# Performance work log

Hardware: AMD Instinct MI355X
Metric: run time of the kernel (lower is better)

## Reference

```python
import jax, jax.numpy as jnp
import numpy as np

B, F, V, D, K = 16384, 39, 30000, 16, 20
EPS = 1e-5


def bn_eval(x, g, b):
    # inference-mode BatchNorm1d with running_mean=0, running_var=1
    return g * x / jnp.sqrt(1.0 + EPS) + b


def setup_inputs() -> dict:
    key = jax.random.key(0)
    ks = jax.random.split(key, 12)
    x = jax.random.randint(ks[0], (B, F), 0, V)
    emb_table = jax.random.normal(ks[1], (F * V, D), dtype=jnp.float32) * 0.05
    w_c = jax.random.normal(ks[2], (F, F * D), dtype=jnp.float32) * 0.05
    w0 = jax.random.normal(ks[3], (1024, F * D), dtype=jnp.float32) * 0.04
    w1 = jax.random.normal(ks[4], (512, 1024), dtype=jnp.float32) * 0.03
    w_out = jax.random.normal(ks[5], (1, 512), dtype=jnp.float32) * 0.04
    return {
        'x': x, 'emb_table': emb_table,
        'w_c': w_c, 'b_c': jnp.zeros((F,)), 'g_c': jnp.ones((F,)), 'be_c': jnp.zeros((F,)),
        'w0': w0, 'b0': jnp.zeros((1024,)), 'g0': jnp.ones((1024,)), 'be0': jnp.zeros((1024,)),
        'w1': w1, 'b1': jnp.zeros((512,)), 'g1': jnp.ones((512,)), 'be1': jnp.zeros((512,)),
        'w_out': w_out, 'b_out': jnp.zeros((1,)),
    }


def reference(x, emb_table, w_c, b_c, g_c, be_c, w0, b0, g0, be0,
              w1, b1, g1, be1, w_out, b_out):
    offsets = jnp.arange(F, dtype=x.dtype) * V          # per-field offsets
    idx = x + offsets[None, :]                          # [B, F]
    emb = emb_table[idx]                                # [B, F, D] gather

    # controller_mlp: flatten (batch, D, F) layout like torch transpose(1,2)
    flat = jnp.transpose(emb, (0, 2, 1)).reshape(B, F * D)
    h = jax.nn.relu(bn_eval(flat @ w_c.T + b_c, g_c, be_c))
    scores = jax.nn.softmax(h, axis=1)                  # [B, F]

    # kmax_pooling: top-k field indices, sorted ascending, gather weights
    _, kidx = jax.lax.top_k(scores, K)
    kidx = jnp.sort(kidx, axis=1)                       # [B, K]
    w = jnp.take_along_axis(scores, kidx, axis=1)       # [B, K]

    # forward_select: gather selected field embeddings, weight them
    sel = jnp.take_along_axis(emb, kidx[:, :, None], axis=1)  # [B, K, D]
    weighted = sel * w[:, :, None]

    # scatter back into full field slots (unselected fields are zero)
    full = jnp.zeros((B, F, D), weighted.dtype)
    bidx = jnp.arange(B)[:, None]
    full = full.at[bidx, kidx].set(weighted)            # [B, F, D]

    z = jnp.transpose(full, (0, 2, 1)).reshape(B, F * D)
    z = jax.nn.relu(bn_eval(z @ w0.T + b0, g0, be0))
    z = jax.nn.relu(bn_eval(z @ w1.T + b1, g1, be1))
    out = jax.nn.sigmoid(z @ w_out.T + b_out)           # [B, 1]
    return out.squeeze(-1)
```

## Files before the change

kernel.cpp:

```cpp
#include <hip/hip_runtime.h>
#include <math.h>

#define B_SZ 16384
#define F_N 39
#define V_N 30000
#define D_N 16
#define K_SEL 20
#define FD 624
#define KP0 640
#define NCP 48
#define N0 1024
#define N1 512
#define CBR 16
#define ALD 648

typedef unsigned short u16;
typedef __attribute__((ext_vector_type(8))) short bf16x8;
typedef __attribute__((ext_vector_type(8))) unsigned short u16x8;
typedef __attribute__((ext_vector_type(4))) float f32x4;
typedef __attribute__((ext_vector_type(4))) unsigned short u16x4;

__device__ __forceinline__ u16 f2bf(float v) {
    union { float f; unsigned u; } x; x.f = v;
    unsigned r = x.u + 0x7fff + ((x.u >> 16) & 1);
    return (u16)(r >> 16);
}
__device__ __forceinline__ float bf2f(u16 v) {
    union { unsigned u; float f; } x; x.u = ((unsigned)v) << 16;
    return x.f;
}
__device__ __forceinline__ unsigned cvtpk2(float a, float b) {
    unsigned d;
    asm("v_cvt_pk_bf16_f32 %0, %1, %2" : "=v"(d) : "v"(a), "v"(b));
    return d;
}

#define GLD16(gp, lp) __builtin_amdgcn_global_load_lds( \
    (const __attribute__((address_space(1))) unsigned int*)(gp), \
    (__attribute__((address_space(3))) unsigned int*)(lp), 16, 0, 0)

#define PREP_W0 (N0 * KP0)
#define PREP_W1 (N1 * N0)
#define PREP_WC (NCP * KP0)
#define PREP_TOT (PREP_W0 + PREP_W1 + PREP_WC + 3 * NCP + B_SZ)

__global__ __launch_bounds__(256) void prep_all_kernel(
    const float* __restrict__ w0, const float* __restrict__ w1,
    const float* __restrict__ w_c, const float* __restrict__ b_c,
    const float* __restrict__ g_c, const float* __restrict__ be_c,
    u16* __restrict__ w0b, u16* __restrict__ w1b, u16* __restrict__ wcb,
    float* __restrict__ bcp, float* __restrict__ gcp, float* __restrict__ becp,
    float* __restrict__ outp)
{
    int i = blockIdx.x * blockDim.x + threadIdx.x;
    if (i < PREP_W0) {
        int n = i / KP0, kk = i - n * KP0;
        float v = 0.f;
        if (kk < FD) v = w0[n * FD + (kk & 15) * F_N + (kk >> 4)];
        w0b[i] = f2bf(v);
        return;
    }
    i -= PREP_W0;
    if (i < PREP_W1) { w1b[i] = f2bf(w1[i]); return; }
    i -= PREP_W1;
    if (i < PREP_WC) {
        int n = i / KP0, kk = i - n * KP0;
        float v = 0.f;
        if (n < F_N && kk < FD) v = w_c[n * FD + (kk & 15) * F_N + (kk >> 4)];
        wcb[i] = f2bf(v);
        return;
    }
    i -= PREP_WC;
    if (i < 3 * NCP) {
        int which = i / NCP, n = i - which * NCP;
        float v = 0.f;
        if (n < F_N) v = (which == 0) ? b_c[n] : (which == 1) ? g_c[n] : be_c[n];
        ((which == 0) ? bcp : (which == 1) ? gcp : becp)[n] = v;
        return;
    }
    i -= 3 * NCP;
    if (i < B_SZ) outp[i] = 0.f;
}

__global__ __launch_bounds__(256) void fused_controller_kernel(
    const int* __restrict__ x, const float* __restrict__ emb_table,
    const u16* __restrict__ wcb, const float* __restrict__ bcp,
    const float* __restrict__ gcp, const float* __restrict__ becp,
    u16* __restrict__ zb)
{
    __shared__ __align__(16) u16 Al[CBR * ALD];
    __shared__ float vv[CBR][49];
    __shared__ f32x4 part[4][64][3];
    __shared__ float selw[CBR][F_N];

    const int t    = threadIdx.x;
    const int wave = t >> 6;
    const int lane = t & 63;
    const int b0   = blockIdx.x * CBR;

    {
        const int p0 = t, p1 = t + 256, p2 = t + 512;
        const int xi0 = x[b0 * F_N + p0];
        const int xi1 = x[b0 * F_N + p1];
        const int xi2 = (p2 < CBR * F_N) ? x[b0 * F_N + p2] : 0;
        const int pp[3] = { p0, p1, p2 };
        const int xx[3] = { xi0, xi1, xi2 };
        #pragma unroll
        for (int s = 0; s < 3; ++s) {
            const int p = pp[s];
            if (p < CBR * F_N) {
                const int row = p / F_N;
                const int f   = p - row * F_N;
                const float4* src =
                    (const float4*)(emb_table + (size_t)(xx[s] + f * V_N) * D_N);
                float4 v0 = src[0], v1 = src[1], v2 = src[2], v3 = src[3];
                uint4 o0 = { cvtpk2(v0.x, v0.y), cvtpk2(v0.z, v0.w),
                             cvtpk2(v1.x, v1.y), cvtpk2(v1.z, v1.w) };
                uint4 o1 = { cvtpk2(v2.x, v2.y), cvtpk2(v2.z, v2.w),
                             cvtpk2(v3.x, v3.y), cvtpk2(v3.z, v3.w) };
                *(uint4*)&Al[row * ALD + f * D_N]     = o0;
                *(uint4*)&Al[row * ALD + f * D_N + 8] = o1;
            }
        }
    }
    __syncthreads();

    const int m = lane & 15;
    const int q = lane >> 4;
    f32x4 acc0 = {}, acc1 = {}, acc2 = {};
    {
        const u16* ap  = &Al[m * ALD + wave * 160 + q * 8];
        const u16* bp0 = wcb + (size_t)(0  + m) * KP0 + wave * 160 + q * 8;
        const u16* bp1 = wcb + (size_t)(16 + m) * KP0 + wave * 160 + q * 8;
        const u16* bp2 = wcb + (size_t)(32 + m) * KP0 + wave * 160 + q * 8;
        #pragma unroll
        for (int k = 0; k < 5; ++k) {
            bf16x8 af = *(const bf16x8*)ap;
            bf16x8 b0 = *(const bf16x8*)bp0;
            bf16x8 b1 = *(const bf16x8*)bp1;
            bf16x8 b2 = *(const bf16x8*)bp2;
            acc0 = __builtin_amdgcn_mfma_f32_16x16x32_bf16(af, b0, acc0, 0, 0, 0);
            acc1 = __builtin_amdgcn_mfma_f32_16x16x32_bf16(af, b1, acc1, 0, 0, 0);
            acc2 = __builtin_amdgcn_mfma_f32_16x16x32_bf16(af, b2, acc2, 0, 0, 0);
            ap += 32; bp0 += 32; bp1 += 32; bp2 += 32;
        }
    }
    part[wave][lane][0] = acc0;
    part[wave][lane][1] = acc1;
    part[wave][lane][2] = acc2;
    __syncthreads();

    {
        f32x4 r0 = part[0][lane][0] + part[1][lane][0] + part[2][lane][0] + part[3][lane][0];
        f32x4 r1 = part[0][lane][1] + part[1][lane][1] + part[2][lane][1] + part[3][lane][1];
        f32x4 r2 = part[0][lane][2] + part[1][lane][2] + part[2][lane][2] + part[3][lane][2];

        const float rs = rsqrtf(1.0f + 1e-5f);
        if (q == wave) {
            #pragma unroll
            for (int j = 0; j < 3; ++j) {
                const f32x4 a = (j == 0) ? r0 : (j == 1) ? r1 : r2;
                const int n = j * 16 + m;
                const float gn = gcp[n] * rs;
                const float bn = becp[n];
                const float bi = bcp[n];
                #pragma unroll
                for (int r = 0; r < 4; ++r)
                    vv[wave * 4 + r][n] = fmaxf(fmaf(gn, a[r] + bi, bn), 0.f);
            }
        }
    }
    __syncthreads();

    {
        const int row = wave * 4 + (lane >> 4);
        const int fl  = lane & 15;
        float e[3] = {0.f, 0.f, 0.f};
        float mloc = -1e30f;
        #pragma unroll
        for (int it = 0; it < 3; ++it) {
            const int f = fl + 16 * it;
            if (f < F_N) { e[it] = vv[row][f]; mloc = fmaxf(mloc, e[it]); }
        }
        mloc = fmaxf(mloc, __shfl_xor(mloc, 1, 64));
        mloc = fmaxf(mloc, __shfl_xor(mloc, 2, 64));
        mloc = fmaxf(mloc, __shfl_xor(mloc, 4, 64));
        mloc = fmaxf(mloc, __shfl_xor(mloc, 8, 64));
        float sloc = 0.f;
        #pragma unroll
        for (int it = 0; it < 3; ++it) {
            const int f = fl + 16 * it;
            if (f < F_N) { e[it] = expf(e[it] - mloc); sloc += e[it]; }
        }
        sloc += __shfl_xor(sloc, 1, 64);
        sloc += __shfl_xor(sloc, 2, 64);
        sloc += __shfl_xor(sloc, 4, 64);
        sloc += __shfl_xor(sloc, 8, 64);
        const float inv = 1.f / sloc;
        #pragma unroll
        for (int it = 0; it < 3; ++it) {
            const int f = fl + 16 * it;
            if (f < F_N) vv[row][f] = e[it];
        }

        int rank[3] = {};
        for (int gg = 0; gg < F_N; ++gg) {
            const float o = vv[row][gg];
            #pragma unroll
            for (int it = 0; it < 3; ++it) {
                const int f = fl + 16 * it;
                if (f < F_N)
                    rank[it] += (o > e[it] || (o == e[it] && gg < f)) ? 1 : 0;
            }
        }
        #pragma unroll
        for (int it = 0; it < 3; ++it) {
            const int f = fl + 16 * it;
            if (f < F_N)
                selw[row][f] = (rank[it] < K_SEL) ? e[it] * inv : 0.f;
        }
    }
    __syncthreads();

    for (int gp = t; gp < CBR * 40; gp += 256) {
        const int row  = gp / 40;
        const int slot = gp - row * 40;
        u16* dst = zb + (size_t)(b0 + row) * KP0 + slot * D_N;
        uint4 o0 = {0u,0u,0u,0u}, o1 = {0u,0u,0u,0u};
        if (slot < F_N) {
            const float w = selw[row][slot];
            u16x8 a0 = *(u16x8*)&Al[row * ALD + slot * D_N];
            u16x8 a1 = *(u16x8*)&Al[row * ALD + slot * D_N + 8];
            o0 = (uint4){ cvtpk2(bf2f(a0[0]) * w, bf2f(a0[1]) * w),
                          cvtpk2(bf2f(a0[2]) * w, bf2f(a0[3]) * w),
                          cvtpk2(bf2f(a0[4]) * w, bf2f(a0[5]) * w),
                          cvtpk2(bf2f(a0[6]) * w, bf2f(a0[7]) * w) };
            o1 = (uint4){ cvtpk2(bf2f(a1[0]) * w, bf2f(a1[1]) * w),
                          cvtpk2(bf2f(a1[2]) * w, bf2f(a1[3]) * w),
                          cvtpk2(bf2f(a1[4]) * w, bf2f(a1[5]) * w),
                          cvtpk2(bf2f(a1[6]) * w, bf2f(a1[7]) * w) };
        }
        *(uint4*)dst       = o0;
        *(uint4*)(dst + 8) = o1;
    }
}

template<int MODE>
__global__ __launch_bounds__(512) void gemm_mfma_bn_relu(
    const u16* __restrict__ A, const u16* __restrict__ W,
    const float* __restrict__ bias, const float* __restrict__ g,
    const float* __restrict__ be, u16* __restrict__ Cout,
    int M, int N, int Kp,
    const float* __restrict__ w_out, float* __restrict__ outp)
{
    __shared__ __align__(16) u16 SM[3 * 12288];

    const int t    = threadIdx.x;
    const int wave = t >> 6;
    const int lane = t & 63;
    const int wm   = wave >> 1, wn = wave & 1;
    const int m0   = blockIdx.x * 256;
    const int n0   = blockIdx.y * 128;

    const int rA0 = t >> 2;
    const int cA0 = (t & 3) ^ ((rA0 >> 1) & 3);
    const int rA1 = 128 + rA0;
    const int cA1 = (t & 3) ^ ((rA1 >> 1) & 3);
    const u16* gA0 = A + (size_t)(m0 + rA0) * Kp + cA0 * 8;
    const u16* gA1 = A + (size_t)(m0 + rA1) * Kp + cA1 * 8;
    const u16* gB  = W + (size_t)(n0 + rA0) * Kp + cA0 * 8;
    const int dA0 = t * 8, dA1 = 4096 + t * 8, dB = 8192 + t * 8;

    const int q    = lane >> 4;
    const int lr16 = lane & 15;

    int aoff[4], boff[4];
    #pragma unroll
    for (int i = 0; i < 4; ++i) {
        int ra = wm * 64 + i * 16 + lr16;
        aoff[i] = ra * 32 + ((q ^ ((ra >> 1) & 3)) * 8);
        int rb = wn * 64 + i * 16 + lr16;
        boff[i] = rb * 32 + ((q ^ ((rb >> 1) & 3)) * 8);
    }

    const int NIT = Kp >> 5;

    GLD16(gA0, SM + dA0);
    GLD16(gA1, SM + dA1);
    GLD16(gB,  SM + dB);
    gA0 += 32; gA1 += 32; gB += 32;
    GLD16(gA0, SM + 12288 + dA0);
    GLD16(gA1, SM + 12288 + dA1);
    GLD16(gB,  SM + 12288 + dB);
    gA0 += 32; gA1 += 32; gB += 32;

    f32x4 acc[4][4] = {};
    int cur = 0, stg = 2;

    for (int it = 0; it < NIT - 1; ++it) {
        asm volatile("s_waitcnt vmcnt(3)" ::: "memory");
        __builtin_amdgcn_s_barrier();
        __builtin_amdgcn_sched_barrier(0);

        if (it + 2 < NIT) {
            u16* s = SM + stg * 12288;
            GLD16(gA0, s + dA0);
            GLD16(gA1, s + dA1);
            GLD16(gB,  s + dB);
            gA0 += 32; gA1 += 32; gB += 32;
        }

        const u16* ac = SM + cur * 12288;
        const u16* bc = ac + 8192;
        bf16x8 af[4], bfr[4];
        #pragma unroll
        for (int i = 0; i < 4; ++i) af[i]  = *(const bf16x8*)(ac + aoff[i]);
        #pragma unroll
        for (int j = 0; j < 4; ++j) bfr[j] = *(const bf16x8*)(bc + boff[j]);

        __builtin_amdgcn_s_setprio(1);
        #pragma unroll
        for (int i = 0; i < 4; ++i)
            #pragma unroll
            for (int j = 0; j < 4; ++j)
                acc[i][j] = __builtin_amdgcn_mfma_f32_16x16x32_bf16(
                    af[i], bfr[j], acc[i][j], 0, 0, 0);
        __builtin_amdgcn_s_setprio(0);

        cur = (cur == 2) ? 0 : cur + 1;
        stg = (stg == 2) ? 0 : stg + 1;
    }

    asm volatile("s_waitcnt vmcnt(0)" ::: "memory");
    __builtin_amdgcn_s_barrier();
    __builtin_amdgcn_sched_barrier(0);
    {
        const u16* ac = SM + cur * 12288;
        const u16* bc = ac + 8192;
        bf16x8 af[4], bfr[4];
        #pragma unroll
        for (int i = 0; i < 4; ++i) af[i]  = *(const bf16x8*)(ac + aoff[i]);
        #pragma unroll
        for (int j = 0; j < 4; ++j) bfr[j] = *(const bf16x8*)(bc + boff[j]);
        __builtin_amdgcn_s_setprio(1);
        #pragma unroll
        for (int i = 0; i < 4; ++i)
            #pragma unroll
            for (int j = 0; j < 4; ++j)
                acc[i][j] = __builtin_amdgcn_mfma_f32_16x16x32_bf16(
                    af[i], bfr[j], acc[i][j], 0, 0, 0);
        __builtin_amdgcn_s_setprio(0);
    }

    const float rs = rsqrtf(1.0f + 1e-5f);
    if (MODE == 0) {
        __syncthreads();
        u16* Cs = SM;
        #pragma unroll
        for (int j = 0; j < 4; ++j) {
            const int nl = wn * 64 + j * 16 + lr16;
            const int n  = n0 + nl;
            const float bn_g = g[n] * rs;
            const float bn_b = be[n];
            const float bi   = bias[n];
            #pragma unroll
            for (int i = 0; i < 4; ++i) {
                const int mlb = wm * 64 + i * 16 + q * 4;
                float v0 = fmaxf(fmaf(bn_g, acc[i][j][0] + bi, bn_b), 0.f);
                float v1 = fmaxf(fmaf(bn_g, acc[i][j][1] + bi, bn_b), 0.f);
                float v2 = fmaxf(fmaf(bn_g, acc[i][j][2] + bi, bn_b), 0.f);
                float v3 = fmaxf(fmaf(bn_g, acc[i][j][3] + bi, bn_b), 0.f);
                unsigned pA = cvtpk2(v0, v1);
                unsigned pB = cvtpk2(v2, v3);
                Cs[(mlb + 0) * 136 + nl] = (u16)pA;
                Cs[(mlb + 1) * 136 + nl] = (u16)(pA >> 16);
                Cs[(mlb + 2) * 136 + nl] = (u16)pB;
                Cs[(mlb + 3) * 136 + nl] = (u16)(pB >> 16);
            }
        }
        __syncthreads();
        #pragma unroll
        for (int s = 0; s < 8; ++s) {
            const int chunk = s * 512 + t;
            const int row   = chunk >> 4;
            const int col   = (chunk & 15) << 3;
            *(u16x8*)&Cout[(size_t)(m0 + row) * N + n0 + col] =
                *(const u16x8*)&Cs[row * 136 + col];
        }
    } else {
        float s[4][4] = {};
        #pragma unroll
        for (int j = 0; j < 4; ++j) {
            const int n = n0 + wn * 64 + j * 16 + lr16;
            const float bn_g = g[n] * rs;
            const float bn_b = be[n];
            const float bi   = bias[n];
            const float wo   = w_out[n];
            #pragma unroll
            for (int i = 0; i < 4; ++i)
                #pragma unroll
                for (int r = 0; r < 4; ++r) {
                    float v = acc[i][j][r] + bi;
                    v = fmaxf(fmaf(bn_g, v, bn_b), 0.f);
                    s[i][r] = fmaf(v, wo, s[i][r]);
                }
        }
        #pragma unroll
        for (int i = 0; i < 4; ++i)
            #pragma unroll
            for (int r = 0; r < 4; ++r) {
                float v = s[i][r];
                v += __shfl_xor(v, 1, 64);
                v += __shfl_xor(v, 2, 64);
                v += __shfl_xor(v, 4, 64);
                v += __shfl_xor(v, 8, 64);
                s[i][r] = v;
            }
        if (lr16 == 0) {
            #pragma unroll
            for (int i = 0; i < 4; ++i) {
                const int mbase = m0 + wm * 64 + i * 16 + q * 4;
                #pragma unroll
                for (int r = 0; r < 4; ++r)
                    atomicAdd(&outp[mbase + r], s[i][r]);
            }
        }
    }
}

__global__ __launch_bounds__(256) void sigmoid_kernel(
    const float* __restrict__ outp, const float* __restrict__ b_out,
    float* __restrict__ out)
{
    const int b = blockIdx.x * 256 + threadIdx.x;
    out[b] = 1.f / (1.f + expf(-(outp[b] + b_out[0])));
}

extern "C" void kernel_launch(void* const* d_in, const int* in_sizes, int n_in,
                              void* d_out, int out_size, void* d_ws, size_t ws_size,
                              hipStream_t stream)
{
    const int*   x     = (const int*)  d_in[0];
    const float* emb   = (const float*)d_in[1];
    const float* w_c   = (const float*)d_in[2];
    const float* b_c   = (const float*)d_in[3];
    const float* g_c   = (const float*)d_in[4];
    const float* be_c  = (const float*)d_in[5];
    const float* w0    = (const float*)d_in[6];
    const float* b0    = (const float*)d_in[7];
    const float* g0    = (const float*)d_in[8];
    const float* be0   = (const float*)d_in[9];
    const float* w1    = (const float*)d_in[10];
    const float* b1    = (const float*)d_in[11];
    const float* g1    = (const float*)d_in[12];
    const float* be1   = (const float*)d_in[13];
    const float* w_out = (const float*)d_in[14];
    const float* b_out = (const float*)d_in[15];
    float* out = (float*)d_out;

    u16*   zb    = (u16*)d_ws;
    u16*   w0b   = zb    + (size_t)B_SZ * KP0;
    u16*   h0b   = w0b   + (size_t)N0 * KP0;
    u16*   w1b   = h0b   + (size_t)B_SZ * N0;
    u16*   wcb   = w1b   + (size_t)N1 * N0;
    float* outp  = (float*)(wcb + (size_t)NCP * KP0);
    float* bcp   = outp + B_SZ;
    float* gcp   = bcp + NCP;
    float* becp  = gcp + NCP;

    prep_all_kernel<<<(PREP_TOT + 255) / 256, 256, 0, stream>>>(
        w0, w1, w_c, b_c, g_c, be_c, w0b, w1b, wcb, bcp, gcp, becp, outp);

    fused_controller_kernel<<<B_SZ / CBR, 256, 0, stream>>>(
        x, emb, wcb, bcp, gcp, becp, zb);

    gemm_mfma_bn_relu<0><<<dim3(B_SZ / 256, N0 / 128), 512, 0, stream>>>(
        zb, w0b, b0, g0, be0, h0b, B_SZ, N0, KP0, nullptr, nullptr);

    gemm_mfma_bn_relu<1><<<dim3(B_SZ / 256, N1 / 128), 512, 0, stream>>>(
        h0b, w1b, b1, g1, be1, nullptr, B_SZ, N1, N0, w_out, outp);

    sigmoid_kernel<<<B_SZ / 256, 256, 0, stream>>>(outp, b_out, out);
}
```

Measured before the change: 207.2 us.

## Vectorize weight prep via LDS transpose and split GEMM MFMA loop into halves

The weight-prep kernel now stages w0/w_c rows in shared memory, reads them coalesced as float4, and writes packed bf16 pairs. The w1 conversion and output zeroing are also vectorized, with a fixed grid of 399 blocks. Separately, the GEMM main loop issues its LDS fragment loads before the next global-to-LDS prefetch and splits the 16 MFMAs into two halves separated by an extra workgroup barrier, trying to overlap LDS reads with compute. The extra barrier per iteration and the explicit lgkmcnt waits could add synchronization stalls.

```diff
diff --git a/kernel.cpp b/kernel.cpp
--- a/kernel.cpp
+++ b/kernel.cpp
@@ -39,11 +39,6 @@
     (const __attribute__((address_space(1))) unsigned int*)(gp), \
     (__attribute__((address_space(3))) unsigned int*)(lp), 16, 0, 0)
 
-#define PREP_W0 (N0 * KP0)
-#define PREP_W1 (N1 * N0)
-#define PREP_WC (NCP * KP0)
-#define PREP_TOT (PREP_W0 + PREP_W1 + PREP_WC + 3 * NCP + B_SZ)
-
 __global__ __launch_bounds__(256) void prep_all_kernel(
     const float* __restrict__ w0, const float* __restrict__ w1,
     const float* __restrict__ w_c, const float* __restrict__ b_c,
@@ -52,34 +47,65 @@
     float* __restrict__ bcp, float* __restrict__ gcp, float* __restrict__ becp,
     float* __restrict__ outp)
 {
-    int i = blockIdx.x * blockDim.x + threadIdx.x;
-    if (i < PREP_W0) {
-        int n = i / KP0, kk = i - n * KP0;
-        float v = 0.f;
-        if (kk < FD) v = w0[n * FD + (kk & 15) * F_N + (kk >> 4)];
-        w0b[i] = f2bf(v);
+    __shared__ float Lb[8][624];
+    const int bid = blockIdx.x;
+    const int t   = threadIdx.x;
+
+    if (bid < 134) {
+        const bool is_w0 = (bid < 128);
+        const int r0 = is_w0 ? bid * 8 : (bid - 128) * 8;
+        const int nrows_src = is_w0 ? N0 : F_N;
+        const float* __restrict__ src = is_w0 ? w0 : w_c;
+        u16* __restrict__ dst = is_w0 ? w0b : wcb;
+
+        for (int j = t; j < 8 * 156; j += 256) {
+            const int row = j / 156;
+            const int c4  = j - row * 156;
+            const int n   = r0 + row;
+            if (n < nrows_src)
+                *(float4*)&Lb[row][c4 * 4] =
+                    *(const float4*)&src[(size_t)n * FD + c4 * 4];
+        }
+        __syncthreads();
+
+        for (int j = t; j < 8 * 320; j += 256) {
+            const int row = j / 320;
+            const int pr  = j - row * 320;
+            const int n   = r0 + row;
+            const int k0  = pr * 2;
+            float v0 = 0.f, v1 = 0.f;
+            if (n < nrows_src) {
+                const int d0 = k0 & 15,       f0 = k0 >> 4;
+                const int d1 = (k0 + 1) & 15, f1 = (k0 + 1) >> 4;
+                if (f0 < F_N) v0 = Lb[row][d0 * F_N + f0];
+                if (f1 < F_N) v1 = Lb[row][d1 * F_N + f1];
+            }
+            *(unsigned*)&dst[(size_t)n * KP0 + k0] = cvtpk2(v0, v1);
+        }
         return;
     }
-    i -= PREP_W0;
-    if (i < PREP_W1) { w1b[i] = f2bf(w1[i]); return; }
-    i -= PREP_W1;
-    if (i < PREP_WC) {
-        int n = i / KP0, kk = i - n * KP0;
-        float v = 0.f;
-        if (n < F_N && kk < FD) v = w_c[n * FD + (kk & 15) * F_N + (kk >> 4)];
-        wcb[i] = f2bf(v);
+    if (bid < 390) {
+        const size_t e0 = (size_t)(bid - 134) * 2048 + t * 8;
+        float4 v0 = *(const float4*)(w1 + e0);
+        float4 v1 = *(const float4*)(w1 + e0 + 4);
+        uint4 o = { cvtpk2(v0.x, v0.y), cvtpk2(v0.z, v0.w),
+                    cvtpk2(v1.x, v1.y), cvtpk2(v1.z, v1.w) };
+        *(uint4*)(w1b + e0) = o;
         return;
     }
-    i -= PREP_WC;
-    if (i < 3 * NCP) {
-        int which = i / NCP, n = i - which * NCP;
+    if (bid < 398) {
+        const size_t e0 = (size_t)(bid - 390) * 2048 + t * 8;
+        float4 z = {0.f, 0.f, 0.f, 0.f};
+        *(float4*)(outp + e0)     = z;
+        *(float4*)(outp + e0 + 4) = z;
+        return;
+    }
+    if (t < 3 * NCP) {
+        const int which = t / NCP, n = t - which * NCP;
         float v = 0.f;
         if (n < F_N) v = (which == 0) ? b_c[n] : (which == 1) ? g_c[n] : be_c[n];
         ((which == 0) ? bcp : (which == 1) ? gcp : becp)[n] = v;
-        return;
-    }
-    i -= 3 * NCP;
-    if (i < B_SZ) outp[i] = 0.f;
+    }
 }
 
 __global__ __launch_bounds__(256) void fused_controller_kernel(
@@ -302,6 +328,16 @@
         __builtin_amdgcn_s_barrier();
         __builtin_amdgcn_sched_barrier(0);
 
+        const u16* ac = SM + cur * 12288;
+        const u16* bc = ac + 8192;
+
+        bf16x8 af0 = *(const bf16x8*)(ac + aoff[0]);
+        bf16x8 af1 = *(const bf16x8*)(ac + aoff[1]);
+        bf16x8 b0v = *(const bf16x8*)(bc + boff[0]);
+        bf16x8 b1v = *(const bf16x8*)(bc + boff[1]);
+        bf16x8 b2v = *(const bf16x8*)(bc + boff[2]);
+        bf16x8 b3v = *(const bf16x8*)(bc + boff[3]);
+
         if (it + 2 < NIT) {
             u16* s = SM + stg * 12288;
             GLD16(gA0, s + dA0);
@@ -310,21 +346,33 @@
             gA0 += 32; gA1 += 32; gB += 32;
         }
 
-        const u16* ac = SM + cur * 12288;
-        const u16* bc = ac + 8192;
-        bf16x8 af[4], bfr[4];
-        #pragma unroll
-        for (int i = 0; i < 4; ++i) af[i]  = *(const bf16x8*)(ac + aoff[i]);
-        #pragma unroll
-        for (int j = 0; j < 4; ++j) bfr[j] = *(const bf16x8*)(bc + boff[j]);
-
+        asm volatile("s_waitcnt lgkmcnt(0)" ::: "memory");
+        __builtin_amdgcn_sched_barrier(0);
         __builtin_amdgcn_s_setprio(1);
-        #pragma unroll
-        for (int i = 0; i < 4; ++i)
-            #pragma unroll
-            for (int j = 0; j < 4; ++j)
-                acc[i][j] = __builtin_amdgcn_mfma_f32_16x16x32_bf16(
-                    af[i], bfr[j], acc[i][j], 0, 0, 0);
+        acc[0][0] = __builtin_amdgcn_mfma_f32_16x16x32_bf16(af0, b0v, acc[0][0], 0, 0, 0);
+        acc[0][1] = __builtin_amdgcn_mfma_f32_16x16x32_bf16(af0, b1v, acc[0][1], 0, 0, 0);
+        acc[0][2] = __builtin_amdgcn_mfma_f32_16x16x32_bf16(af0, b2v, acc[0][2], 0, 0, 0);
+        acc[0][3] = __builtin_amdgcn_mfma_f32_16x16x32_bf16(af0, b3v, acc[0][3], 0, 0, 0);
+        acc[1][0] = __builtin_amdgcn_mfma_f32_16x16x32_bf16(af1, b0v, acc[1][0], 0, 0, 0);
+        acc[1][1] = __builtin_amdgcn_mfma_f32_16x16x32_bf16(af1, b1v, acc[1][1], 0, 0, 0);
+        acc[1][2] = __builtin_amdgcn_mfma_f32_16x16x32_bf16(af1, b2v, acc[1][2], 0, 0, 0);
+        acc[1][3] = __builtin_amdgcn_mfma_f32_16x16x32_bf16(af1, b3v, acc[1][3], 0, 0, 0);
+        __builtin_amdgcn_s_setprio(0);
+        __builtin_amdgcn_s_barrier();
+
+        bf16x8 af2 = *(const bf16x8*)(ac + aoff[2]);
+        bf16x8 af3 = *(const bf16x8*)(ac + aoff[3]);
+        asm volatile("s_waitcnt lgkmcnt(0)" ::: "memory");
+        __builtin_amdgcn_sched_barrier(0);
+        __builtin_amdgcn_s_setprio(1);
+        acc[2][0] = __builtin_amdgcn_mfma_f32_16x16x32_bf16(af2, b0v, acc[2][0], 0, 0, 0);
+        acc[2][1] = __builtin_amdgcn_mfma_f32_16x16x32_bf16(af2, b1v, acc[2][1], 0, 0, 0);
+        acc[2][2] = __builtin_amdgcn_mfma_f32_16x16x32_bf16(af2, b2v, acc[2][2], 0, 0, 0);
+        acc[2][3] = __builtin_amdgcn_mfma_f32_16x16x32_bf16(af2, b3v, acc[2][3], 0, 0, 0);
+        acc[3][0] = __builtin_amdgcn_mfma_f32_16x16x32_bf16(af3, b0v, acc[3][0], 0, 0, 0);
+        acc[3][1] = __builtin_amdgcn_mfma_f32_16x16x32_bf16(af3, b1v, acc[3][1], 0, 0, 0);
+        acc[3][2] = __builtin_amdgcn_mfma_f32_16x16x32_bf16(af3, b2v, acc[3][2], 0, 0, 0);
+        acc[3][3] = __builtin_amdgcn_mfma_f32_16x16x32_bf16(af3, b3v, acc[3][3], 0, 0, 0);
         __builtin_amdgcn_s_setprio(0);
 
         cur = (cur == 2) ? 0 : cur + 1;
@@ -468,7 +516,7 @@
     float* gcp   = bcp + NCP;
     float* becp  = gcp + NCP;
 
-    prep_all_kernel<<<(PREP_TOT + 255) / 256, 256, 0, stream>>>(
+    prep_all_kernel<<<399, 256, 0, stream>>>(
         w0, w1, w_c, b_c, g_c, be_c, w0b, w1b, wcb, bcp, gcp, becp, outp);
 
     fused_controller_kernel<<<B_SZ / CBR, 256, 0, stream>>>(
```

Measured after the change: 205.6 us. Within noise of the previous version (-0.8%).
